# Kernel tuning notes

Hardware: AMD Instinct MI355X
Metric: run time of the kernel (lower is better)

## Reference

```python
import jax, jax.numpy as jnp
import numpy as np

G, M, K = 4096, 50, 30          # graphs, nodes per graph, sort-pool k
H, NUM_LAYERS, F_IN = 32, 3, 128
DEG = 8
N = G * M
E = N * DEG
D_LAT = H * NUM_LAYERS + 1       # 97 = conv1d kernel/stride
DENSE_DIM = (((K - 2) // 2 + 1) - 5 + 1) * 32  # 352


def setup_inputs() -> dict:
    key = jax.random.key(0)
    ks = jax.random.split(key, 14)
    x = jax.random.normal(ks[0], (N, F_IN), dtype=jnp.float32)
    # graph-local random edges so each subgraph is self-contained
    offs = (jnp.arange(E, dtype=jnp.int32) // (M * DEG)) * M
    src = jax.random.randint(ks[1], (E,), 0, M, dtype=jnp.int32) + offs
    dst = jax.random.randint(ks[2], (E,), 0, M, dtype=jnp.int32) + offs
    edge_index = jnp.stack([src, dst])
    batch = jnp.repeat(jnp.arange(G, dtype=jnp.int32), M)

    def lin(k, i, o):
        return (jax.random.normal(k, (i, o), dtype=jnp.float32) / np.sqrt(i)).astype(jnp.float32)

    W0, b0 = lin(ks[3], F_IN, H), jnp.zeros((H,), jnp.float32)
    W1, b1 = lin(ks[4], H, H), jnp.zeros((H,), jnp.float32)
    W2, b2 = lin(ks[5], H, H), jnp.zeros((H,), jnp.float32)
    W3, b3 = lin(ks[6], H, 1), jnp.zeros((1,), jnp.float32)
    C1w = (jax.random.normal(ks[7], (16, 1, D_LAT)) / np.sqrt(D_LAT)).astype(jnp.float32)
    C1b = jnp.zeros((16,), jnp.float32)
    C2w = (jax.random.normal(ks[8], (32, 16, 5)) / np.sqrt(16 * 5)).astype(jnp.float32)
    C2b = jnp.zeros((32,), jnp.float32)
    L1w, L1b = lin(ks[9], DENSE_DIM, 128), jnp.zeros((128,), jnp.float32)
    L2w, L2b = lin(ks[10], 128, 1), jnp.zeros((1,), jnp.float32)
    return {"x": x, "edge_index": edge_index, "batch": batch,
            "W0": W0, "b0": b0, "W1": W1, "b1": b1, "W2": W2, "b2": b2,
            "W3": W3, "b3": b3, "C1w": C1w, "C1b": C1b, "C2w": C2w, "C2b": C2b,
            "L1w": L1w, "L1b": L1b, "L2w": L2w, "L2b": L2b}


def _gcn_norm(edge_index, n):
    # add self loops, symmetric normalization (PyG GCNConv default)
    loop = jnp.arange(n, dtype=edge_index.dtype)
    src = jnp.concatenate([edge_index[0], loop])
    dst = jnp.concatenate([edge_index[1], loop])
    deg = jax.ops.segment_sum(jnp.ones_like(dst, dtype=jnp.float32), dst, num_segments=n)
    dinv = jnp.where(deg > 0, deg ** -0.5, 0.0)
    return src, dst, dinv[src] * dinv[dst]


def _gcn_conv(h, W, b, src, dst, norm, n):
    h = h @ W                                    # [N, out]
    msg = h[src] * norm[:, None]                 # gather + weight
    return jax.ops.segment_sum(msg, dst, num_segments=n) + b


def reference(x, edge_index, batch, W0, b0, W1, b1, W2, b2, W3, b3,
              C1w, C1b, C2w, C2b, L1w, L1b, L2w, L2b):
    n = x.shape[0]
    src, dst, norm = _gcn_norm(edge_index, n)
    h1 = jnp.tanh(_gcn_conv(x, W0, b0, src, dst, norm, n))
    h2 = jnp.tanh(_gcn_conv(h1, W1, b1, src, dst, norm, n))
    h3 = jnp.tanh(_gcn_conv(h2, W2, b2, src, dst, norm, n))
    h4 = jnp.tanh(_gcn_conv(h3, W3, b3, src, dst, norm, n))
    lat = jnp.concatenate([h1, h2, h3, h4], axis=-1)      # [N, 97]
    # global_sort_pool: graphs are contiguous equal-size blocks (batch = arange(G).repeat(M)),
    # sort nodes within each graph by last channel, descending, keep top K
    xd = lat.reshape(G, M, D_LAT)
    order = jnp.argsort(-xd[..., -1], axis=1)             # [G, M]
    xs = jnp.take_along_axis(xd, order[..., None], axis=1)[:, :K]  # [G, K, 97]
    # Conv1d(1,16,97,stride=97) on [G,1,K*97] == per-slot linear over the 97 latent dims
    z = jnp.einsum('gtd,cd->gct', xs, C1w[:, 0, :]) + C1b[None, :, None]  # [G,16,K]
    z = jax.nn.relu(z)
    z = z.reshape(G, 16, K // 2, 2).max(axis=-1)          # MaxPool1d(2,2) -> [G,16,15]
    z = jax.lax.conv_general_dilated(z, C2w, window_strides=(1,), padding='VALID',
                                     dimension_numbers=('NCH', 'OIH', 'NCH'))
    z = jax.nn.relu(z + C2b[None, :, None])               # [G,32,11]
    z = z.reshape(G, -1)                                  # [G,352]
    z = jax.nn.relu(z @ L1w + L1b)
    # dropout: eval mode (identity)
    return z @ L2w + L2b                                  # [G,1]
```

## Files before the change

### kernel.cpp

```cpp
#include <hip/hip_runtime.h>
#include <math.h>

#define NG 4096
#define M 50
#define KTOP 30
#define H 32
#define F_IN 128
#define EPG 400
#define PADE 552
#define E_TOTAL (NG * EPG)
#define DLAT 97
#define LATS 100
#define NTHREADS 256
#define WS_C1P 0

__device__ __forceinline__ float fast_tanh(float x) {
    x = fminf(fmaxf(x, -15.f), 15.f);
    float e = __expf(2.f * x);
    return 1.f - 2.f / (e + 1.f);
}

__global__ void prep_kernel(const float* __restrict__ C1w, float* __restrict__ ws) {
    const int tid = blockIdx.x * blockDim.x + threadIdx.x;
    if (tid < 1600) {
        int c = tid / 100, d = tid - c * 100;
        ws[WS_C1P + tid] = (d < DLAT) ? C1w[c * DLAT + d] : 0.f;
    }
}

template <int KIN>
__device__ __forceinline__ void gcn_matmul(const float* hin, int istride,
                                           const float* __restrict__ W,
                                           float (*tb)[H], int tid) {
    const int j = tid & 31, iset = tid >> 5;
    float acc[7];
    int rows[7];
#pragma unroll
    for (int r = 0; r < 7; r++) {
        acc[r] = 0.f;
        int i = iset + r * 8;
        rows[r] = (i >= M) ? (M - 1) : i;
    }
#pragma unroll 2
    for (int k4 = 0; k4 < KIN / 4; k4++) {
        const float w0 = W[(4 * k4 + 0) * H + j];
        const float w1 = W[(4 * k4 + 1) * H + j];
        const float w2 = W[(4 * k4 + 2) * H + j];
        const float w3 = W[(4 * k4 + 3) * H + j];
#pragma unroll
        for (int r = 0; r < 7; r++) {
            const float4 xv = *(const float4*)(hin + rows[r] * istride + 4 * k4);
            acc[r] += xv.x * w0 + xv.y * w1 + xv.z * w2 + xv.w * w3;
        }
    }
#pragma unroll
    for (int r = 0; r < 7; r++) {
        int i = iset + r * 8;
        if (i < M) tb[i][j] = acc[r];
    }
}

__device__ __forceinline__ void gcn_agg(const float (*tbuf)[H], const float* __restrict__ b,
                                        float (*lat)[LATS], int col0,
                                        const float* dinv, const unsigned short* csr_off,
                                        const unsigned char* csr_src, const float* csr_nrm,
                                        int tid) {
    const int j = tid & 31, iset = tid >> 5;
    for (int i = iset; i < M; i += 8) {
        float acc = tbuf[i][j] * dinv[i] * dinv[i];
        int e0 = csr_off[i], e1 = csr_off[i + 1];
        for (int e = e0; e < e1; e += 4) {
            unsigned sp = *(const unsigned*)(csr_src + e);
            float4 nr = *(const float4*)(csr_nrm + e);
            acc += tbuf[sp & 255][j] * nr.x;
            acc += tbuf[(sp >> 8) & 255][j] * nr.y;
            acc += tbuf[(sp >> 16) & 255][j] * nr.z;
            acc += tbuf[sp >> 24][j] * nr.w;
        }
        lat[i][col0 + j] = fast_tanh(acc + b[j]);
    }
}

struct Post {
    float pbuf[16][15];
    union {
        struct { float z1[16][KTOP]; unsigned char ord[52]; } a;
        struct { float z2[352]; float red[256]; } b;
    } u;
};

__global__ __launch_bounds__(NTHREADS, 4)
void dgcnn_kernel(const float* __restrict__ x, const int* __restrict__ eidx,
                  const float* __restrict__ ws,
                  const float* __restrict__ W0, const float* __restrict__ b0,
                  const float* __restrict__ W1, const float* __restrict__ b1,
                  const float* __restrict__ W2, const float* __restrict__ b2,
                  const float* __restrict__ W3, const float* __restrict__ b3,
                  const float* __restrict__ C1b,
                  const float* __restrict__ C2w, const float* __restrict__ C2b,
                  const float* __restrict__ L1w, const float* __restrict__ L1b,
                  const float* __restrict__ L2w, const float* __restrict__ L2b,
                  float* __restrict__ out) {
    __shared__ __align__(16) union Big {
        float xs[M][F_IN];
        struct { float lat[M][LATS]; Post post; } s;
    } big;
    __shared__ __align__(16) float tbuf[M][H];
    __shared__ __align__(16) float csr_nrm[PADE];
    __shared__ unsigned char csr_src[PADE];
    __shared__ unsigned short csr_off[M + 2];
    __shared__ int   degi[M];
    __shared__ float dinv[M];

    const int g = blockIdx.x;
    const int tid = threadIdx.x;
    const int nbase = g * M;
    const int ebase = g * EPG;

    {
        const float4* xg4 = (const float4*)(x + (size_t)nbase * F_IN);
        float4* xs4 = (float4*)big.xs;
        for (int idx = tid; idx < M * F_IN / 4; idx += NTHREADS)
            xs4[idx] = xg4[idx];
    }
    if (tid < M) degi[tid] = 1;
    for (int idx = tid; idx < PADE; idx += NTHREADS) {
        csr_nrm[idx] = 0.f;
        csr_src[idx] = 0;
    }
    __syncthreads();
    for (int e = tid; e < EPG; e += NTHREADS) {
        int d = eidx[E_TOTAL + ebase + e] - nbase;
        atomicAdd(&degi[d], 1);
    }
    __syncthreads();
    if (tid < M) dinv[tid] = rsqrtf((float)degi[tid]);
    if (tid < 64) {
        int cnt  = (tid < M) ? (degi[tid] - 1) : 0;
        int cntp = (cnt + 3) & ~3;
        int incl = cntp;
#pragma unroll
        for (int off = 1; off < 64; off <<= 1) {
            int nv = __shfl_up(incl, off);
            if (tid >= off) incl += nv;
        }
        if (tid < M) {
            csr_off[tid] = (unsigned short)(incl - cntp);
            degi[tid] = incl - cntp;
        }
        if (tid == M - 1) csr_off[M] = (unsigned short)incl;
    }
    __syncthreads();
    for (int e = tid; e < EPG; e += NTHREADS) {
        int s = eidx[ebase + e] - nbase;
        int d = eidx[E_TOTAL + ebase + e] - nbase;
        float nr = dinv[s] * dinv[d];
        int pos = atomicAdd(&degi[d], 1);
        csr_src[pos] = (unsigned char)s;
        csr_nrm[pos] = nr;
    }
    gcn_matmul<F_IN>(&big.xs[0][0], F_IN, W0, tbuf, tid);
    __syncthreads();

    gcn_agg(tbuf, b0, big.s.lat, 0, dinv, csr_off, csr_src, csr_nrm, tid);
    for (int idx = tid; idx < 3 * M; idx += NTHREADS)
        big.s.lat[idx / 3][DLAT + idx % 3] = 0.f;
    __syncthreads();
    gcn_matmul<H>(&big.s.lat[0][0], LATS, W1, tbuf, tid);
    __syncthreads();
    gcn_agg(tbuf, b1, big.s.lat, 32, dinv, csr_off, csr_src, csr_nrm, tid);
    __syncthreads();
    gcn_matmul<H>(&big.s.lat[0][32], LATS, W2, tbuf, tid);
    __syncthreads();
    gcn_agg(tbuf, b2, big.s.lat, 64, dinv, csr_off, csr_src, csr_nrm, tid);
    __syncthreads();
    if (tid < M) {
        float acc = 0.f;
        for (int k = 0; k < H; k++) acc += big.s.lat[tid][64 + k] * W3[k];
        tbuf[tid][0] = acc;
    }
    __syncthreads();
    if (tid < M) {
        float acc = tbuf[tid][0] * dinv[tid] * dinv[tid];
        int e0 = csr_off[tid], e1 = csr_off[tid + 1];
        for (int e = e0; e < e1; e += 4) {
            unsigned sp = *(const unsigned*)(csr_src + e);
            float4 nr = *(const float4*)(csr_nrm + e);
            acc += tbuf[sp & 255][0] * nr.x + tbuf[(sp >> 8) & 255][0] * nr.y
                 + tbuf[(sp >> 16) & 255][0] * nr.z + tbuf[sp >> 24][0] * nr.w;
        }
        big.s.lat[tid][96] = tanhf(acc + b3[0]);
    }
    __syncthreads();

    if (tid < M) {
        float v = big.s.lat[tid][96];
        int r = 0;
        for (int jj = 0; jj < M; jj++) {
            float vj = big.s.lat[jj][96];
            r += (vj > v) || (vj == v && jj < tid);
        }
        big.s.post.u.a.ord[r] = (unsigned char)tid;
    }
    __syncthreads();

    for (int idx = tid; idx < 16 * KTOP; idx += NTHREADS) {
        int t = idx >> 4, c = idx & 15;
        const float4* row = (const float4*)big.s.lat[big.s.post.u.a.ord[t]];
        const float4* cw  = (const float4*)(ws + WS_C1P + c * LATS);
        float acc = 0.f;
#pragma unroll 5
        for (int q = 0; q < LATS / 4; q++) {
            float4 rv = row[q], wv = cw[q];
            acc += rv.x * wv.x + rv.y * wv.y + rv.z * wv.z + rv.w * wv.w;
        }
        big.s.post.u.a.z1[c][t] = fmaxf(acc + C1b[c], 0.f);
    }
    __syncthreads();

    for (int idx = tid; idx < 16 * 15; idx += NTHREADS) {
        int c = idx / 15, t = idx - c * 15;
        big.s.post.pbuf[c][t] = fmaxf(big.s.post.u.a.z1[c][2 * t],
                                      big.s.post.u.a.z1[c][2 * t + 1]);
    }
    __syncthreads();

    for (int idx = tid; idx < 352; idx += NTHREADS) {
        int o = idx / 11, t = idx - o * 11;
        float acc = C2b[o];
        for (int i = 0; i < 16; i++) {
#pragma unroll
            for (int k = 0; k < 5; k++)
                acc += big.s.post.pbuf[i][t + k] * C2w[(o * 16 + i) * 5 + k];
        }
        big.s.post.u.b.z2[idx] = fmaxf(acc, 0.f);
    }
    __syncthreads();

    {
        int jj = tid & 127, half = tid >> 7;
        float acc = (half == 0) ? L1b[jj] : 0.f;
        int f0 = half * 176;
        for (int f = f0; f < f0 + 176; f++)
            acc += big.s.post.u.b.z2[f] * L1w[f * 128 + jj];
        big.s.post.u.b.red[tid] = acc;
    }
    __syncthreads();
    if (tid < 128)
        big.s.post.u.b.red[tid] =
            fmaxf(big.s.post.u.b.red[tid] + big.s.post.u.b.red[tid + 128], 0.f)
            * L2w[tid];
    __syncthreads();
    if (tid < 64) {
        float v = big.s.post.u.b.red[tid] + big.s.post.u.b.red[tid + 64];
#pragma unroll
        for (int off = 32; off >= 1; off >>= 1)
            v += __shfl_down(v, off);
        if (tid == 0) out[g] = v + L2b[0];
    }
}

extern "C" void kernel_launch(void* const* d_in, const int* in_sizes, int n_in,
                              void* d_out, int out_size, void* d_ws, size_t ws_size,
                              hipStream_t stream) {
    const float* x    = (const float*)d_in[0];
    const int*   eidx = (const int*)d_in[1];
    float* ws = (float*)d_ws;
    prep_kernel<<<7, 256, 0, stream>>>((const float*)d_in[11], ws);
    dgcnn_kernel<<<NG, NTHREADS, 0, stream>>>(
        x, eidx, ws,
        (const float*)d_in[3],  (const float*)d_in[4],
        (const float*)d_in[5],  (const float*)d_in[6],
        (const float*)d_in[7],  (const float*)d_in[8],
        (const float*)d_in[9],  (const float*)d_in[10],
        (const float*)d_in[12],
        (const float*)d_in[13], (const float*)d_in[14],
        (const float*)d_in[15], (const float*)d_in[16],
        (const float*)d_in[17], (const float*)d_in[18],
        (float*)d_out);
}
```

Baseline: 375.3 us.

## Stage layer-0 input in two halves and alias post buffers to cut LDS

The first GCN layer's input features are now loaded into shared memory in two 64-column halves, with partial matmul accumulators held in registers across the halves. The post-processing scratch is moved into a union with tbuf, so the big shared buffer only needs to hold the larger of the half-x tile and the latent matrix. This shrinks per-block LDS so more blocks can be resident per CU, which should help hide latency. The cost is an extra barrier and a second global load phase that cannot overlap with the first matmul half.

Measured after the change: 376.7 us. Within noise of the previous version (+0.4%).

```diff
diff --git a/kernel.cpp b/kernel.cpp
--- a/kernel.cpp
+++ b/kernel.cpp
@@ -13,6 +13,7 @@
 #define LATS 100
 #define NTHREADS 256
 #define WS_C1P 0
+#define XH 64
 
 __device__ __forceinline__ float fast_tanh(float x) {
     x = fminf(fmaxf(x, -15.f), 15.f);
@@ -25,6 +26,24 @@
     if (tid < 1600) {
         int c = tid / 100, d = tid - c * 100;
         ws[WS_C1P + tid] = (d < DLAT) ? C1w[c * DLAT + d] : 0.f;
+    }
+}
+
+template <int KIN>
+__device__ __forceinline__ void gcn_matmul_acc(const float* hin, int istride,
+                                               const float* __restrict__ W,
+                                               const int* rows, float* acc, int j) {
+#pragma unroll 2
+    for (int k4 = 0; k4 < KIN / 4; k4++) {
+        const float w0 = W[(4 * k4 + 0) * H + j];
+        const float w1 = W[(4 * k4 + 1) * H + j];
+        const float w2 = W[(4 * k4 + 2) * H + j];
+        const float w3 = W[(4 * k4 + 3) * H + j];
+#pragma unroll
+        for (int r = 0; r < 7; r++) {
+            const float4 xv = *(const float4*)(hin + rows[r] * istride + 4 * k4);
+            acc[r] += xv.x * w0 + xv.y * w1 + xv.z * w2 + xv.w * w3;
+        }
     }
 }
 
@@ -41,18 +60,7 @@
         int i = iset + r * 8;
         rows[r] = (i >= M) ? (M - 1) : i;
     }
-#pragma unroll 2
-    for (int k4 = 0; k4 < KIN / 4; k4++) {
-        const float w0 = W[(4 * k4 + 0) * H + j];
-        const float w1 = W[(4 * k4 + 1) * H + j];
-        const float w2 = W[(4 * k4 + 2) * H + j];
-        const float w3 = W[(4 * k4 + 3) * H + j];
-#pragma unroll
-        for (int r = 0; r < 7; r++) {
-            const float4 xv = *(const float4*)(hin + rows[r] * istride + 4 * k4);
-            acc[r] += xv.x * w0 + xv.y * w1 + xv.z * w2 + xv.w * w3;
-        }
-    }
+    gcn_matmul_acc<KIN>(hin, istride, W, rows, acc, j);
 #pragma unroll
     for (int r = 0; r < 7; r++) {
         int i = iset + r * 8;
@@ -102,10 +110,13 @@
                   const float* __restrict__ L2w, const float* __restrict__ L2b,
                   float* __restrict__ out) {
     __shared__ __align__(16) union Big {
-        float xs[M][F_IN];
-        struct { float lat[M][LATS]; Post post; } s;
+        float xs[M][XH];
+        float lat[M][LATS];
     } big;
-    __shared__ __align__(16) float tbuf[M][H];
+    __shared__ __align__(16) union TP {
+        float tbuf[M][H];
+        Post post;
+    } tp;
     __shared__ __align__(16) float csr_nrm[PADE];
     __shared__ unsigned char csr_src[PADE];
     __shared__ unsigned short csr_off[M + 2];
@@ -120,8 +131,10 @@
     {
         const float4* xg4 = (const float4*)(x + (size_t)nbase * F_IN);
         float4* xs4 = (float4*)big.xs;
-        for (int idx = tid; idx < M * F_IN / 4; idx += NTHREADS)
-            xs4[idx] = xg4[idx];
+        for (int idx = tid; idx < M * XH / 4; idx += NTHREADS) {
+            int i = idx >> 4, q = idx & 15;
+            xs4[idx] = xg4[i * 32 + q];
+        }
     }
     if (tid < M) degi[tid] = 1;
     for (int idx = tid; idx < PADE; idx += NTHREADS) {
@@ -151,6 +164,15 @@
         if (tid == M - 1) csr_off[M] = (unsigned short)incl;
     }
     __syncthreads();
+    const int j1 = tid & 31, iset1 = tid >> 5;
+    float acc1[7];
+    int rows1[7];
+#pragma unroll
+    for (int r = 0; r < 7; r++) {
+        acc1[r] = 0.f;
+        int i = iset1 + r * 8;
+        rows1[r] = (i >= M) ? (M - 1) : i;
+    }
     for (int e = tid; e < EPG; e += NTHREADS) {
         int s = eidx[ebase + e] - nbase;
         int d = eidx[E_TOTAL + ebase + e] - nbase;
@@ -159,54 +181,70 @@
         csr_src[pos] = (unsigned char)s;
         csr_nrm[pos] = nr;
     }
-    gcn_matmul<F_IN>(&big.xs[0][0], F_IN, W0, tbuf, tid);
-    __syncthreads();
-
-    gcn_agg(tbuf, b0, big.s.lat, 0, dinv, csr_off, csr_src, csr_nrm, tid);
+    gcn_matmul_acc<XH>(&big.xs[0][0], XH, W0, rows1, acc1, j1);
+    __syncthreads();
+    {
+        const float4* xg4 = (const float4*)(x + (size_t)nbase * F_IN);
+        float4* xs4 = (float4*)big.xs;
+        for (int idx = tid; idx < M * XH / 4; idx += NTHREADS) {
+            int i = idx >> 4, q = idx & 15;
+            xs4[idx] = xg4[i * 32 + 16 + q];
+        }
+    }
+    __syncthreads();
+    gcn_matmul_acc<XH>(&big.xs[0][0], XH, W0 + XH * H, rows1, acc1, j1);
+#pragma unroll
+    for (int r = 0; r < 7; r++) {
+        int i = iset1 + r * 8;
+        if (i < M) tp.tbuf[i][j1] = acc1[r];
+    }
+    __syncthreads();
+
+    gcn_agg(tp.tbuf, b0, big.lat, 0, dinv, csr_off, csr_src, csr_nrm, tid);
     for (int idx = tid; idx < 3 * M; idx += NTHREADS)
-        big.s.lat[idx / 3][DLAT + idx % 3] = 0.f;
-    __syncthreads();
-    gcn_matmul<H>(&big.s.lat[0][0], LATS, W1, tbuf, tid);
-    __syncthreads();
-    gcn_agg(tbuf, b1, big.s.lat, 32, dinv, csr_off, csr_src, csr_nrm, tid);
-    __syncthreads();
-    gcn_matmul<H>(&big.s.lat[0][32], LATS, W2, tbuf, tid);
-    __syncthreads();
-    gcn_agg(tbuf, b2, big.s.lat, 64, dinv, csr_off, csr_src, csr_nrm, tid);
+        big.lat[idx / 3][DLAT + idx % 3] = 0.f;
+    __syncthreads();
+    gcn_matmul<H>(&big.lat[0][0], LATS, W1, tp.tbuf, tid);
+    __syncthreads();
+    gcn_agg(tp.tbuf, b1, big.lat, 32, dinv, csr_off, csr_src, csr_nrm, tid);
+    __syncthreads();
+    gcn_matmul<H>(&big.lat[0][32], LATS, W2, tp.tbuf, tid);
+    __syncthreads();
+    gcn_agg(tp.tbuf, b2, big.lat, 64, dinv, csr_off, csr_src, csr_nrm, tid);
     __syncthreads();
     if (tid < M) {
         float acc = 0.f;
-        for (int k = 0; k < H; k++) acc += big.s.lat[tid][64 + k] * W3[k];
-        tbuf[tid][0] = acc;
+        for (int k = 0; k < H; k++) acc += big.lat[tid][64 + k] * W3[k];
+        tp.tbuf[tid][0] = acc;
     }
     __syncthreads();
     if (tid < M) {
-        float acc = tbuf[tid][0] * dinv[tid] * dinv[tid];
+        float acc = tp.tbuf[tid][0] * dinv[tid] * dinv[tid];
         int e0 = csr_off[tid], e1 = csr_off[tid + 1];
         for (int e = e0; e < e1; e += 4) {
             unsigned sp = *(const unsigned*)(csr_src + e);
             float4 nr = *(const float4*)(csr_nrm + e);
-            acc += tbuf[sp & 255][0] * nr.x + tbuf[(sp >> 8) & 255][0] * nr.y
-                 + tbuf[(sp >> 16) & 255][0] * nr.z + tbuf[sp >> 24][0] * nr.w;
-        }
-        big.s.lat[tid][96] = tanhf(acc + b3[0]);
+            acc += tp.tbuf[sp & 255][0] * nr.x + tp.tbuf[(sp >> 8) & 255][0] * nr.y
+                 + tp.tbuf[(sp >> 16) & 255][0] * nr.z + tp.tbuf[sp >> 24][0] * nr.w;
+        }
+        big.lat[tid][96] = tanhf(acc + b3[0]);
     }
     __syncthreads();
 
     if (tid < M) {
-        float v = big.s.lat[tid][96];
+        float v = big.lat[tid][96];
         int r = 0;
         for (int jj = 0; jj < M; jj++) {
-            float vj = big.s.lat[jj][96];
+            float vj = big.lat[jj][96];
             r += (vj > v) || (vj == v && jj < tid);
         }
-        big.s.post.u.a.ord[r] = (unsigned char)tid;
+        tp.post.u.a.ord[r] = (unsigned char)tid;
     }
     __syncthreads();
 
     for (int idx = tid; idx < 16 * KTOP; idx += NTHREADS) {
         int t = idx >> 4, c = idx & 15;
-        const float4* row = (const float4*)big.s.lat[big.s.post.u.a.ord[t]];
+        const float4* row = (const float4*)big.lat[tp.post.u.a.ord[t]];
         const float4* cw  = (const float4*)(ws + WS_C1P + c * LATS);
         float acc = 0.f;
 #pragma unroll 5
@@ -214,14 +252,14 @@
             float4 rv = row[q], wv = cw[q];
             acc += rv.x * wv.x + rv.y * wv.y + rv.z * wv.z + rv.w * wv.w;
         }
-        big.s.post.u.a.z1[c][t] = fmaxf(acc + C1b[c], 0.f);
+        tp.post.u.a.z1[c][t] = fmaxf(acc + C1b[c], 0.f);
     }
     __syncthreads();
 
     for (int idx = tid; idx < 16 * 15; idx += NTHREADS) {
         int c = idx / 15, t = idx - c * 15;
-        big.s.post.pbuf[c][t] = fmaxf(big.s.post.u.a.z1[c][2 * t],
-                                      big.s.post.u.a.z1[c][2 * t + 1]);
+        tp.post.pbuf[c][t] = fmaxf(tp.post.u.a.z1[c][2 * t],
+                                   tp.post.u.a.z1[c][2 * t + 1]);
     }
     __syncthreads();
 
@@ -231,9 +269,9 @@
         for (int i = 0; i < 16; i++) {
 #pragma unroll
             for (int k = 0; k < 5; k++)
-                acc += big.s.post.pbuf[i][t + k] * C2w[(o * 16 + i) * 5 + k];
-        }
-        big.s.post.u.b.z2[idx] = fmaxf(acc, 0.f);
+                acc += tp.post.pbuf[i][t + k] * C2w[(o * 16 + i) * 5 + k];
+        }
+        tp.post.u.b.z2[idx] = fmaxf(acc, 0.f);
     }
     __syncthreads();
 
@@ -242,17 +280,17 @@
         float acc = (half == 0) ? L1b[jj] : 0.f;
         int f0 = half * 176;
         for (int f = f0; f < f0 + 176; f++)
-            acc += big.s.post.u.b.z2[f] * L1w[f * 128 + jj];
-        big.s.post.u.b.red[tid] = acc;
+            acc += tp.post.u.b.z2[f] * L1w[f * 128 + jj];
+        tp.post.u.b.red[tid] = acc;
     }
     __syncthreads();
     if (tid < 128)
-        big.s.post.u.b.red[tid] =
-            fmaxf(big.s.post.u.b.red[tid] + big.s.post.u.b.red[tid + 128], 0.f)
+        tp.post.u.b.red[tid] =
+            fmaxf(tp.post.u.b.red[tid] + tp.post.u.b.red[tid + 128], 0.f)
             * L2w[tid];
     __syncthreads();
     if (tid < 64) {
-        float v = big.s.post.u.b.red[tid] + big.s.post.u.b.red[tid + 64];
+        float v = tp.post.u.b.red[tid] + tp.post.u.b.red[tid + 64];
 #pragma unroll
         for (int off = 32; off >= 1; off >>= 1)
             v += __shfl_down(v, off);
```
